# Optimization experiments

Measured on AMD Instinct MI355X. Metric: run time of the kernel, lower is better.

The kernel has to match this reference:

```python
import jax, jax.numpy as jnp
import numpy as np

N_NODES = 50000
N_EDGES = 500000
D = 128  # node/edge feature dim


def setup_inputs() -> dict:
    key = jax.random.key(0)
    k1, k2, k3, k4, k5 = jax.random.split(key, 5)
    x_node = jax.random.normal(k1, (N_NODES, D), dtype=jnp.float32)
    x_edge = jax.random.normal(k2, (N_EDGES, D), dtype=jnp.float32)
    edge_index = jax.random.randint(k3, (N_EDGES, 2), 0, N_NODES, dtype=jnp.int64)
    # MLP params: Linear(3D -> D) -> ReLU -> Linear(D -> D)
    W1 = jax.random.normal(k4, (3 * D, D), dtype=jnp.float32) * (1.0 / np.sqrt(3 * D))
    b1 = jnp.zeros((D,), dtype=jnp.float32)
    W2 = jax.random.normal(k5, (D, D), dtype=jnp.float32) * (1.0 / np.sqrt(D))
    b2 = jnp.zeros((D,), dtype=jnp.float32)
    return {"x_node": x_node, "x_edge": x_edge, "edge_index": edge_index,
            "W1": W1, "b1": b1, "W2": W2, "b2": b2}


def reference(x_node, x_edge, edge_index, W1, b1, W2, b2):
    # gather node features at both endpoints of each edge
    v0 = x_node[edge_index[:, 0]]          # [E, D]
    v1 = x_node[edge_index[:, 1]]          # [E, D]
    x_new = jnp.concatenate([v0, v1, x_edge], axis=1)  # [E, 3D]
    h = jax.nn.relu(x_new @ W1 + b1)       # [E, D]
    x_edge_new = h @ W2 + b2               # [E, D]
    return x_edge_new
```

## Files before the change

kernel.cpp:

```cpp
#include <hip/hip_runtime.h>
#include <stdint.h>

#define D 128
#define MT 64

typedef short short8 __attribute__((ext_vector_type(8)));
typedef float f32x16 __attribute__((ext_vector_type(16)));

__device__ __forceinline__ unsigned short f2bf(float f) {
    union { float f; uint32_t u; } v;
    v.f = f;
    uint32_t u = v.u;
    uint32_t r = (u + 0x7fffu + ((u >> 16) & 1u)) >> 16;
    return (unsigned short)r;
}

__global__ void pack_weights_kernel(const float* __restrict__ W1,
                                    const float* __restrict__ W2,
                                    unsigned short* __restrict__ W1p,
                                    unsigned short* __restrict__ W2p) {
    int t = blockIdx.x * 256 + threadIdx.x;
    if (t < 6144) {
        int kt = t >> 8, nt = (t >> 6) & 3, lane = t & 63;
        int n = nt * 32 + (lane & 31);
        int kb = kt * 16 + (lane >> 5) * 8;
        unsigned short* dst = W1p + t * 8;
        #pragma unroll
        for (int j = 0; j < 8; ++j) dst[j] = f2bf(W1[(kb + j) * D + n]);
    } else if (t < 8192) {
        int u = t - 6144;
        int kt = u >> 8, nt = (u >> 6) & 3, lane = u & 63;
        int n = nt * 32 + (lane & 31);
        int kb = kt * 16 + (lane >> 5) * 8;
        unsigned short* dst = W2p + u * 8;
        #pragma unroll
        for (int j = 0; j < 8; ++j) dst[j] = f2bf(W2[(kb + j) * D + n]);
    }
}

__global__ __launch_bounds__(512, 6) void edge_mlp_kernel(
    const float* __restrict__ x_node,
    const float* __restrict__ x_edge,
    const int* __restrict__ eidx,
    const unsigned short* __restrict__ W1p,
    const unsigned short* __restrict__ W2p,
    const float* __restrict__ b1,
    const float* __restrict__ b2,
    float* __restrict__ out,
    int E) {
    __shared__ unsigned short lds[MT * 392];
    unsigned short* Hs = lds;

    const int t = threadIdx.x;
    const int r0 = blockIdx.x * MT;

    {
        const int lane32 = t & 31;
        const int rsub = t >> 5;
        #pragma unroll
        for (int rb = 0; rb < 4; ++rb) {
            int row = rb * 16 + rsub;
            int rg = r0 + row;
            int rgc = rg < E ? rg : E - 1;
            int e0 = eidx[2 * rgc];
            int e1 = eidx[2 * rgc + 1];
            float4 v0 = ((const float4*)(x_node + (size_t)e0 * D))[lane32];
            float4 v1 = ((const float4*)(x_node + (size_t)e1 * D))[lane32];
            float4 v2 = ((const float4*)(x_edge + (size_t)rgc * D))[lane32];
            unsigned short* base = &lds[row * 392 + lane32 * 4];
            ushort4 p;
            p.x = f2bf(v0.x); p.y = f2bf(v0.y); p.z = f2bf(v0.z); p.w = f2bf(v0.w);
            *(ushort4*)(base) = p;
            p.x = f2bf(v1.x); p.y = f2bf(v1.y); p.z = f2bf(v1.z); p.w = f2bf(v1.w);
            *(ushort4*)(base + 128) = p;
            p.x = f2bf(v2.x); p.y = f2bf(v2.y); p.z = f2bf(v2.z); p.w = f2bf(v2.w);
            *(ushort4*)(base + 256) = p;
        }
    }
    __syncthreads();

    const int w = t >> 6;
    const int cb = w & 3;
    const int rt = w >> 2;
    const int lane = t & 63;
    const int lrow = lane & 31;
    const int khalf = (lane >> 5) * 8;
    const int n = cb * 32 + lrow;
    const int rbump = (lane >> 5) * 4;
    const int arow = rt * 32 + lrow;

    f32x16 acc;
    #pragma unroll
    for (int i = 0; i < 16; ++i) acc[i] = 0.f;

    for (int kt = 0; kt < 24; ++kt) {
        short8 a = *(const short8*)&lds[arow * 392 + kt * 16 + khalf];
        short8 b = *(const short8*)(W1p + ((kt * 4 + cb) * 64 + lane) * 8);
        acc = __builtin_amdgcn_mfma_f32_32x32x16_bf16(a, b, acc, 0, 0, 0);
    }
    __syncthreads();

    {
        float b1v = b1[n];
        #pragma unroll
        for (int r = 0; r < 16; ++r) {
            int rr = rt * 32 + (r & 3) + 8 * (r >> 2) + rbump;
            Hs[rr * 136 + n] = f2bf(fmaxf(acc[r] + b1v, 0.f));
        }
    }
    __syncthreads();

    f32x16 c;
    #pragma unroll
    for (int i = 0; i < 16; ++i) c[i] = 0.f;

    #pragma unroll
    for (int kt = 0; kt < 8; ++kt) {
        short8 a = *(const short8*)&Hs[arow * 136 + kt * 16 + khalf];
        short8 b = *(const short8*)(W2p + ((kt * 4 + cb) * 64 + lane) * 8);
        c = __builtin_amdgcn_mfma_f32_32x32x16_bf16(a, b, c, 0, 0, 0);
    }

    {
        float b2v = b2[n];
        #pragma unroll
        for (int r = 0; r < 16; ++r) {
            int rr = rt * 32 + (r & 3) + 8 * (r >> 2) + rbump;
            int rg = r0 + rr;
            if (rg < E) out[(size_t)rg * D + n] = c[r] + b2v;
        }
    }
}

extern "C" void kernel_launch(void* const* d_in, const int* in_sizes, int n_in,
                              void* d_out, int out_size, void* d_ws, size_t ws_size,
                              hipStream_t stream) {
    const float* x_node = (const float*)d_in[0];
    const float* x_edge = (const float*)d_in[1];
    const int*   eidx   = (const int*)d_in[2];
    const float* W1     = (const float*)d_in[3];
    const float* b1     = (const float*)d_in[4];
    const float* W2     = (const float*)d_in[5];
    const float* b2     = (const float*)d_in[6];
    float* out = (float*)d_out;

    const int E = in_sizes[1] / D;

    unsigned short* W1p = (unsigned short*)d_ws;
    unsigned short* W2p = W1p + 6144 * 8;

    pack_weights_kernel<<<32, 256, 0, stream>>>(W1, W2, W1p, W2p);

    int nblk = (E + MT - 1) / MT;
    edge_mlp_kernel<<<nblk, 512, 0, stream>>>(x_node, x_edge, eidx, W1p, W2p, b1, b2, out, E);
}
```

Measured before the change: 520.5 us.

## Batch gather loads and software-prefetch weight fragments ahead of MFMA loops

The gather phase now issues all edge-index loads first, then all 12 float4 feature loads, then the bf16 conversion and LDS stores, so more global loads are in flight per thread. The first four W1 fragments are loaded before the gather and refilled four k-steps ahead inside the fully unrolled first GEMM loop. All eight W2 fragments are loaded before the barrier that precedes the second GEMM. The aim is to hide global-load latency behind other work, at the cost of extra VGPRs, which may cut occupancy under launch_bounds(512,6) or cause spills.

```diff
diff --git a/kernel.cpp b/kernel.cpp
--- a/kernel.cpp
+++ b/kernel.cpp
@@ -54,31 +54,6 @@
     const int t = threadIdx.x;
     const int r0 = blockIdx.x * MT;
 
-    {
-        const int lane32 = t & 31;
-        const int rsub = t >> 5;
-        #pragma unroll
-        for (int rb = 0; rb < 4; ++rb) {
-            int row = rb * 16 + rsub;
-            int rg = r0 + row;
-            int rgc = rg < E ? rg : E - 1;
-            int e0 = eidx[2 * rgc];
-            int e1 = eidx[2 * rgc + 1];
-            float4 v0 = ((const float4*)(x_node + (size_t)e0 * D))[lane32];
-            float4 v1 = ((const float4*)(x_node + (size_t)e1 * D))[lane32];
-            float4 v2 = ((const float4*)(x_edge + (size_t)rgc * D))[lane32];
-            unsigned short* base = &lds[row * 392 + lane32 * 4];
-            ushort4 p;
-            p.x = f2bf(v0.x); p.y = f2bf(v0.y); p.z = f2bf(v0.z); p.w = f2bf(v0.w);
-            *(ushort4*)(base) = p;
-            p.x = f2bf(v1.x); p.y = f2bf(v1.y); p.z = f2bf(v1.z); p.w = f2bf(v1.w);
-            *(ushort4*)(base + 128) = p;
-            p.x = f2bf(v2.x); p.y = f2bf(v2.y); p.z = f2bf(v2.z); p.w = f2bf(v2.w);
-            *(ushort4*)(base + 256) = p;
-        }
-    }
-    __syncthreads();
-
     const int w = t >> 6;
     const int cb = w & 3;
     const int rt = w >> 2;
@@ -89,15 +64,69 @@
     const int rbump = (lane >> 5) * 4;
     const int arow = rt * 32 + lrow;
 
+    const unsigned short* bp1 = W1p + ((size_t)cb * 64 + lane) * 8;
+    const unsigned short* bp2 = W2p + ((size_t)cb * 64 + lane) * 8;
+
+    short8 bbuf0 = *(const short8*)(bp1);
+    short8 bbuf1 = *(const short8*)(bp1 + 1 * 2048);
+    short8 bbuf2 = *(const short8*)(bp1 + 2 * 2048);
+    short8 bbuf3 = *(const short8*)(bp1 + 3 * 2048);
+
+    {
+        const int lane32 = t & 31;
+        const int rsub = t >> 5;
+
+        int2 e[4];
+        int rgc[4];
+        #pragma unroll
+        for (int rb = 0; rb < 4; ++rb) {
+            int rg = r0 + rb * 16 + rsub;
+            rgc[rb] = rg < E ? rg : E - 1;
+            e[rb] = ((const int2*)eidx)[rgc[rb]];
+        }
+        float4 v0[4], v1[4], v2[4];
+        #pragma unroll
+        for (int rb = 0; rb < 4; ++rb) {
+            v0[rb] = ((const float4*)(x_node + (size_t)e[rb].x * D))[lane32];
+            v1[rb] = ((const float4*)(x_node + (size_t)e[rb].y * D))[lane32];
+            v2[rb] = ((const float4*)(x_edge + (size_t)rgc[rb] * D))[lane32];
+        }
+        #pragma unroll
+        for (int rb = 0; rb < 4; ++rb) {
+            int row = rb * 16 + rsub;
+            unsigned short* base = &lds[row * 392 + lane32 * 4];
+            ushort4 p;
+            p.x = f2bf(v0[rb].x); p.y = f2bf(v0[rb].y); p.z = f2bf(v0[rb].z); p.w = f2bf(v0[rb].w);
+            *(ushort4*)(base) = p;
+            p.x = f2bf(v1[rb].x); p.y = f2bf(v1[rb].y); p.z = f2bf(v1[rb].z); p.w = f2bf(v1[rb].w);
+            *(ushort4*)(base + 128) = p;
+            p.x = f2bf(v2[rb].x); p.y = f2bf(v2[rb].y); p.z = f2bf(v2[rb].z); p.w = f2bf(v2[rb].w);
+            *(ushort4*)(base + 256) = p;
+        }
+    }
+    __syncthreads();
+
     f32x16 acc;
     #pragma unroll
     for (int i = 0; i < 16; ++i) acc[i] = 0.f;
 
+    #pragma unroll
     for (int kt = 0; kt < 24; ++kt) {
         short8 a = *(const short8*)&lds[arow * 392 + kt * 16 + khalf];
-        short8 b = *(const short8*)(W1p + ((kt * 4 + cb) * 64 + lane) * 8);
+        short8 b;
+        switch (kt & 3) {
+            case 0: b = bbuf0; if (kt + 4 < 24) bbuf0 = *(const short8*)(bp1 + (kt + 4) * 2048); break;
+            case 1: b = bbuf1; if (kt + 4 < 24) bbuf1 = *(const short8*)(bp1 + (kt + 4) * 2048); break;
+            case 2: b = bbuf2; if (kt + 4 < 24) bbuf2 = *(const short8*)(bp1 + (kt + 4) * 2048); break;
+            default: b = bbuf3; if (kt + 4 < 24) bbuf3 = *(const short8*)(bp1 + (kt + 4) * 2048); break;
+        }
         acc = __builtin_amdgcn_mfma_f32_32x32x16_bf16(a, b, acc, 0, 0, 0);
     }
+
+    short8 b2buf[8];
+    #pragma unroll
+    for (int i = 0; i < 8; ++i) b2buf[i] = *(const short8*)(bp2 + i * 2048);
+
     __syncthreads();
 
     {
@@ -117,8 +146,7 @@
     #pragma unroll
     for (int kt = 0; kt < 8; ++kt) {
         short8 a = *(const short8*)&Hs[arow * 136 + kt * 16 + khalf];
-        short8 b = *(const short8*)(W2p + ((kt * 4 + cb) * 64 + lane) * 8);
-        c = __builtin_amdgcn_mfma_f32_32x32x16_bf16(a, b, c, 0, 0, 0);
+        c = __builtin_amdgcn_mfma_f32_32x32x16_bf16(a, b2buf[kt], c, 0, 0, 0);
     }
 
     {
```

New measurement: 533.4 us. 1.02x slower.
